# Kernel tuning notes

Hardware: AMD Instinct MI355X
Metric: run time of the kernel (lower is better)

The kernel has to match this reference:

```python
import jax, jax.numpy as jnp
import numpy as np

B, T, A, S = 8, 64, 4, 512
V, EXT_V = 32000, 33000  # base vocab, base + OOV extensions


def setup_inputs() -> dict:
    key = jax.random.key(0)
    k1, k2, k3, k4, k5 = jax.random.split(key, 5)
    vocab_probs = jax.random.uniform(k1, (B, T, V), dtype=jnp.float32)
    vocab_probs = vocab_probs / vocab_probs.sum(-1, keepdims=True)
    generation_probs = jax.random.uniform(k2, (B, T, A), dtype=jnp.float32)
    agentwise_attn = jax.random.uniform(k3, (B, T, A, S), dtype=jnp.float32)
    agentwise_attn = agentwise_attn / agentwise_attn.sum(-1, keepdims=True)
    agent_attn = jax.random.uniform(k4, (B, T, A), dtype=jnp.float32)
    agent_attn = agent_attn / agent_attn.sum(-1, keepdims=True)
    article = jax.random.randint(k5, (B, A, S), 0, EXT_V, dtype=jnp.int64)
    return {
        "vocab_probs": vocab_probs,
        "generation_probs": generation_probs,
        "agentwise_attn": agentwise_attn,
        "agent_attn": agent_attn,
        "article": article,
    }


def reference(vocab_probs, generation_probs, agentwise_attn, agent_attn, article):
    # vocab_probs: [B,T,V], generation_probs/agent_attn: [B,T,A],
    # agentwise_attn: [B,T,A,S], article: [B,A,S] int indices < EXT_V
    gen = generation_probs[..., None]                       # [B,T,A,1]
    voc_gen = gen * vocab_probs[:, :, None, :]              # [B,T,A,V]
    copy = (1.0 - gen) * agentwise_attn                     # [B,T,A,S]
    # concat-with-zeros pad to extended vocab
    ext = jnp.concatenate(
        [voc_gen, jnp.zeros((B, T, A, EXT_V - V), voc_gen.dtype)], axis=-1
    )                                                       # [B,T,A,EXT_V]
    # scatter_add copy probs at article token positions (expanded over tgt_len)
    idx = jnp.broadcast_to(article[:, None, :, :], (B, T, A, S))
    bi = jnp.arange(B)[:, None, None, None]
    ti = jnp.arange(T)[None, :, None, None]
    ai = jnp.arange(A)[None, None, :, None]
    ext = ext.at[bi, ti, ai, idx].add(copy)
    # agent-attention weighted sum over agents
    return jnp.einsum("bta,btav->btv", agent_attn, ext)     # [B,T,EXT_V]
```

## Files before the change

### kernel.cpp

```cpp
#include <hip/hip_runtime.h>
#include <hip/hip_bf16.h>

constexpr int B = 8, T = 64, A = 4, S = 512;
constexpr int V = 32000, EXT_V = 33000;
constexpr int V4 = V / 4;
constexpr int E4 = EXT_V / 4;
constexpr int NTHREADS = 1024;

__global__ void __launch_bounds__(NTHREADS, 1)
fused_kernel(const float* __restrict__ vocab,
             const float* __restrict__ gen,
             const float* __restrict__ attn,
             const float* __restrict__ agent_attn,
             const int* __restrict__ article,
             float* __restrict__ out) {
    __shared__ float smem[EXT_V];
    const int bt = blockIdx.x;
    const int b = bt / T;
    const int tid = threadIdx.x;

    float4* s4 = reinterpret_cast<float4*>(smem);
    for (int i = tid; i < E4; i += NTHREADS)
        s4[i] = make_float4(0.f, 0.f, 0.f, 0.f);

    float coef = 0.f;
#pragma unroll
    for (int a = 0; a < A; ++a)
        coef += agent_attn[bt * A + a] * gen[bt * A + a];

    __syncthreads();

#pragma unroll
    for (int k = 0; k < (A * S) / NTHREADS; ++k) {
        const int j = tid + k * NTHREADS;
        const int a = j >> 9;
        const int s = j & (S - 1);
        const int bta = bt * A + a;
        const float g = gen[bta];
        const float w = agent_attn[bta] * (1.0f - g);
        const int idx = article[(b * A + a) * S + s];
        const float val = w * attn[(size_t)bta * S + s];
        atomicAdd(smem + idx, val);
    }
    __syncthreads();

    const float4* __restrict__ vrow = reinterpret_cast<const float4*>(vocab + (size_t)bt * V);
    float4* __restrict__ orow = reinterpret_cast<float4*>(out + (size_t)bt * EXT_V);
    for (int i = tid; i < E4; i += NTHREADS) {
        float4 r = s4[i];
        if (i < V4) {
            const float4 x = vrow[i];
            r.x += x.x * coef;
            r.y += x.y * coef;
            r.z += x.z * coef;
            r.w += x.w * coef;
        }
        orow[i] = r;
    }
}

extern "C" void kernel_launch(void* const* d_in, const int* in_sizes, int n_in,
                              void* d_out, int out_size, void* d_ws, size_t ws_size,
                              hipStream_t stream) {
    const float* vocab      = (const float*)d_in[0];
    const float* gen        = (const float*)d_in[1];
    const float* attn       = (const float*)d_in[2];
    const float* agent_attn = (const float*)d_in[3];
    const int*   article    = (const int*)d_in[4];
    float* out = (float*)d_out;

    fused_kernel<<<B * T, NTHREADS, 0, stream>>>(vocab, gen, attn, agent_attn, article, out);
}
```

Baseline: 128.3 us.

## Split each output row into vocab quarters across smaller blocks for occupancy

```diff
diff --git a/kernel.cpp b/kernel.cpp
--- a/kernel.cpp
+++ b/kernel.cpp
@@ -4,58 +4,89 @@
 constexpr int B = 8, T = 64, A = 4, S = 512;
 constexpr int V = 32000, EXT_V = 33000;
 constexpr int V4 = V / 4;
-constexpr int E4 = EXT_V / 4;
-constexpr int NTHREADS = 1024;
+constexpr int QLEN = 8256;
+constexpr int Q4 = QLEN / 4;
+constexpr int NTH = 512;
+constexpr int NBLK = 4 * B * T;
 
-__global__ void __launch_bounds__(NTHREADS, 1)
+__global__ void __launch_bounds__(NTH, 8)
 fused_kernel(const float* __restrict__ vocab,
              const float* __restrict__ gen,
              const float* __restrict__ attn,
              const float* __restrict__ agent_attn,
              const int* __restrict__ article,
              float* __restrict__ out) {
-    __shared__ float smem[EXT_V];
-    const int bt = blockIdx.x;
+    __shared__ float smem[QLEN];
+    constexpr int PER_XCD = NBLK / 8;
+    const int l = (blockIdx.x & 7) * PER_XCD + (blockIdx.x >> 3);
+    const int bt = l >> 2;
+    const int q  = l & 3;
+    const int vbase = q * QLEN;
+    const int vlen  = (q == 3) ? (EXT_V - 3 * QLEN) : QLEN;
+    const int vlen4 = vlen >> 2;
     const int b = bt / T;
     const int tid = threadIdx.x;
 
+    int   sidx[4];
+    float sval[4];
+#pragma unroll
+    for (int k = 0; k < A; ++k) {
+        sidx[k] = article[(b * A + k) * S + tid] - vbase;
+        sval[k] = attn[(size_t)(bt * A + k) * S + tid];
+    }
+    float coef = 0.f;
+    float wA[4];
+#pragma unroll
+    for (int k = 0; k < A; ++k) {
+        const float g  = gen[bt * A + k];
+        const float aa = agent_attn[bt * A + k];
+        coef += aa * g;
+        wA[k] = aa * (1.0f - g);
+    }
+#pragma unroll
+    for (int k = 0; k < A; ++k) sval[k] *= wA[k];
+
+    const float4* __restrict__ vrow = reinterpret_cast<const float4*>(vocab + (size_t)bt * V);
+    const int g4base = vbase >> 2;
+    float4 p[4];
+#pragma unroll
+    for (int k = 0; k < 4; ++k) {
+        const int gi = g4base + tid + k * NTH;
+        p[k] = (gi < V4) ? vrow[gi] : make_float4(0.f, 0.f, 0.f, 0.f);
+    }
+    const int irem = 4 * NTH + tid;
+    const bool has_rem = irem < vlen4;
+    float4 prem = make_float4(0.f, 0.f, 0.f, 0.f);
+    if (has_rem && (g4base + irem) < V4) prem = vrow[g4base + irem];
+
     float4* s4 = reinterpret_cast<float4*>(smem);
-    for (int i = tid; i < E4; i += NTHREADS)
-        s4[i] = make_float4(0.f, 0.f, 0.f, 0.f);
-
-    float coef = 0.f;
 #pragma unroll
-    for (int a = 0; a < A; ++a)
-        coef += agent_attn[bt * A + a] * gen[bt * A + a];
-
+    for (int k = 0; k < 4; ++k)
+        s4[tid + k * NTH] = make_float4(0.f, 0.f, 0.f, 0.f);
+    if (tid < Q4 - 4 * NTH)
+        s4[4 * NTH + tid] = make_float4(0.f, 0.f, 0.f, 0.f);
     __syncthreads();
 
 #pragma unroll
-    for (int k = 0; k < (A * S) / NTHREADS; ++k) {
-        const int j = tid + k * NTHREADS;
-        const int a = j >> 9;
-        const int s = j & (S - 1);
-        const int bta = bt * A + a;
-        const float g = gen[bta];
-        const float w = agent_attn[bta] * (1.0f - g);
-        const int idx = article[(b * A + a) * S + s];
-        const float val = w * attn[(size_t)bta * S + s];
-        atomicAdd(smem + idx, val);
-    }
+    for (int k = 0; k < A; ++k)
+        if ((unsigned)sidx[k] < (unsigned)vlen)
+            atomicAdd(smem + sidx[k], sval[k]);
     __syncthreads();
 
-    const float4* __restrict__ vrow = reinterpret_cast<const float4*>(vocab + (size_t)bt * V);
     float4* __restrict__ orow = reinterpret_cast<float4*>(out + (size_t)bt * EXT_V);
-    for (int i = tid; i < E4; i += NTHREADS) {
+#pragma unroll
+    for (int k = 0; k < 4; ++k) {
+        const int i = tid + k * NTH;
         float4 r = s4[i];
-        if (i < V4) {
-            const float4 x = vrow[i];
-            r.x += x.x * coef;
-            r.y += x.y * coef;
-            r.z += x.z * coef;
-            r.w += x.w * coef;
-        }
-        orow[i] = r;
+        r.x += p[k].x * coef; r.y += p[k].y * coef;
+        r.z += p[k].z * coef; r.w += p[k].w * coef;
+        orow[g4base + i] = r;
+    }
+    if (has_rem) {
+        float4 r = s4[irem];
+        r.x += prem.x * coef; r.y += prem.y * coef;
+        r.z += prem.z * coef; r.w += prem.w * coef;
+        orow[g4base + irem] = r;
     }
 }
 
@@ -69,5 +100,5 @@
     const int*   article    = (const int*)d_in[4];
     float* out = (float*)d_out;
 
-    fused_kernel<<<B * T, NTHREADS, 0, stream>>>(vocab, gen, attn, agent_attn, article, out);
+    fused_kernel<<<NBLK, NTH, 0, stream>>>(vocab, gen, attn, agent_attn, article, out);
 }
```

Measured after the change: 121.6 us. 5.2% less time.
